# Kernel optimization log

Hardware: AMD Instinct MI355X
Metric: run time of the kernel (lower is better)

The kernel has to match this reference:

```python
import jax, jax.numpy as jnp
import numpy as np

S, B, D, H, DFF = 1024, 8, 1024, 16, 4096
HD = D // H
EPS = 1e-5


def layernorm(x, g, b):
    m = jnp.mean(x, axis=-1, keepdims=True)
    v = jnp.mean(jnp.square(x - m), axis=-1, keepdims=True)
    return (x - m) * jax.lax.rsqrt(v + EPS) * g + b


def setup_inputs() -> dict:
    key = jax.random.key(0)
    ks = jax.random.split(key, 6)
    w = 0.02
    return {
        "src": jax.random.normal(ks[0], (S, B, D), dtype=jnp.float32),
        "in_proj_w": jax.random.normal(ks[1], (3 * D, D), dtype=jnp.float32) * w,
        "in_proj_b": jnp.zeros((3 * D,), dtype=jnp.float32),
        "out_w": jax.random.normal(ks[2], (D, D), dtype=jnp.float32) * w,
        "out_b": jnp.zeros((D,), dtype=jnp.float32),
        "lin1_w": jax.random.normal(ks[3], (DFF, D), dtype=jnp.float32) * w,
        "lin1_b": jnp.zeros((DFF,), dtype=jnp.float32),
        "lin2_w": jax.random.normal(ks[4], (D, DFF), dtype=jnp.float32) * w,
        "lin2_b": jnp.zeros((D,), dtype=jnp.float32),
        "n1_g": jnp.ones((D,), dtype=jnp.float32),
        "n1_b": jnp.zeros((D,), dtype=jnp.float32),
        "n2_g": jnp.ones((D,), dtype=jnp.float32),
        "n2_b": jnp.zeros((D,), dtype=jnp.float32),
    }


def reference(src, in_proj_w, in_proj_b, out_w, out_b,
              lin1_w, lin1_b, lin2_w, lin2_b,
              n1_g, n1_b, n2_g, n2_b):
    # self-attention block (eval mode: dropout = identity)
    qkv = jnp.einsum('sbd,ed->sbe', src, in_proj_w) + in_proj_b  # [S,B,3D]
    q, k, v = jnp.split(qkv, 3, axis=-1)
    q = q.reshape(S, B, H, HD) * (1.0 / np.sqrt(HD)).astype(np.float32)
    k = k.reshape(S, B, H, HD)
    v = v.reshape(S, B, H, HD)
    scores = jnp.einsum('sbhd,tbhd->bhst', q, k)        # [B,H,S,S]
    attn = jax.nn.softmax(scores, axis=-1)
    o = jnp.einsum('bhst,tbhd->sbhd', attn, v).reshape(S, B, D)
    o = jnp.einsum('sbd,ed->sbe', o, out_w) + out_b
    # post-LN residuals
    x = layernorm(src + o, n1_g, n1_b)
    h = jax.nn.relu(jnp.einsum('sbd,fd->sbf', x, lin1_w) + lin1_b)
    f = jnp.einsum('sbf,df->sbd', h, lin2_w) + lin2_b
    return layernorm(x + f, n2_g, n2_b)
```

## Files before the change

kernel.cpp:

```cpp
#include <hip/hip_runtime.h>
#include <cstdint>
#include <cstddef>

#define S_  1024
#define B_  8
#define D_  1024
#define H_  16
#define HD_ 64
#define DFF_ 4096
#define M_  (S_*B_)
#define QKV_N (3*D_)

typedef float f32x4 __attribute__((ext_vector_type(4)));
typedef __bf16 bf16x8 __attribute__((ext_vector_type(8)));
typedef __bf16 bf16x4 __attribute__((ext_vector_type(4)));

#define GLDS16(gp, lp) __builtin_amdgcn_global_load_lds( \
    (__attribute__((address_space(1))) void*)(gp), \
    (__attribute__((address_space(3))) void*)(lp), 16, 0, 0)

#define CB0 (M_*D_/4)
#define CB1 (CB0 + QKV_N*D_/4)
#define CB2 (CB1 + D_*D_/4)
#define CB3 (CB2 + DFF_*D_/4)
#define CB4 (CB3 + D_*DFF_/4)

__global__ __launch_bounds__(256)
void cvt_all(const float* __restrict__ src, const float* __restrict__ w1f,
             const float* __restrict__ w2f, const float* __restrict__ w3f,
             const float* __restrict__ w4f,
             __bf16* __restrict__ src_bf, __bf16* __restrict__ w1,
             __bf16* __restrict__ w2, __bf16* __restrict__ w3,
             __bf16* __restrict__ w4)
{
    int i = blockIdx.x * 256 + threadIdx.x;
    const float* in; __bf16* out; int off;
    if      (i < CB0) { in = src; out = src_bf; off = 0;   }
    else if (i < CB1) { in = w1f; out = w1;     off = CB0; }
    else if (i < CB2) { in = w2f; out = w2;     off = CB1; }
    else if (i < CB3) { in = w3f; out = w3;     off = CB2; }
    else if (i < CB4) { in = w4f; out = w4;     off = CB3; }
    else return;
    int j = i - off;
    float4 v = *(const float4*)(in + (size_t)j * 4);
    __bf16 t[4] = {(__bf16)v.x, (__bf16)v.y, (__bf16)v.z, (__bf16)v.w};
    *(uint2*)(out + (size_t)j * 4) = *(uint2*)t;
}

template<bool OUT_BF16, bool RELU, bool ADD_BIAS, bool SPLITZ>
__global__ __launch_bounds__(512, 2)
void gemm256(const __bf16* __restrict__ A, const __bf16* __restrict__ W,
             const float* __restrict__ bias,
             void* __restrict__ Cv0, void* __restrict__ Cv1,
             int N, int Kloop, int lda)
{
    extern __shared__ __bf16 lds[];

    const int tid  = threadIdx.x;
    const int lane = tid & 63;
    const int wv   = tid >> 6;
    const int quad = lane >> 4;
    const int l15  = lane & 15;
    const int wm   = (wv >> 2) * 128;
    const int wn   = (wv & 3) * 64;

    const int id  = blockIdx.y * gridDim.x + blockIdx.x;
    const int nwg = gridDim.x * gridDim.y;
    const int q8  = nwg >> 3;
    const int k   = (id & 7) * q8 + (id >> 3);
    const int within = k & 31;
    const int chunk  = k >> 5;
    const int nchm   = gridDim.x >> 3;
    const int cm     = chunk % nchm;
    const int cn     = chunk / nchm;
    const int m0 = (cm * 8 + (within & 7)) * 256;
    const int n0 = (cn * 4 + (within >> 3)) * 256;

    void* Cv = Cv0;
    if (SPLITZ) {
        const int koff = blockIdx.z * Kloop;
        A += koff;
        W += koff;
        if (blockIdx.z) Cv = Cv1;
    }

    const int nt = Kloop >> 5;

    const int crow = tid >> 2;
    const int csl  = (tid & 3) ^ ((crow >> 1) & 3);
    const __bf16* gA0 = A + (size_t)(m0 + crow) * lda + csl * 8;
    const __bf16* gA1 = gA0 + (size_t)128 * lda;
    const __bf16* gW0 = W + (size_t)(n0 + crow) * lda + csl * 8;
    const __bf16* gW1 = gW0 + (size_t)128 * lda;
    char* ldsSt = (char*)lds + tid * 16;

    #define STAGE(kt, buf) do { \
        const int ko = (kt) << 5; \
        char* d_ = ldsSt + (buf) * 32768; \
        GLDS16(gW0 + ko, d_ + 16384); \
        GLDS16(gW1 + ko, d_ + 24576); \
        GLDS16(gA0 + ko, d_); \
        GLDS16(gA1 + ko, d_ + 8192); \
    } while (0)

    const int swz = (quad ^ ((l15 >> 1) & 3)) * 8;
    const __bf16* aBase = lds + (wm + l15) * 32 + swz;
    const __bf16* bBase = lds + 8192 + (wn + l15) * 32 + swz;

    #define RDA_ALL(arr, buf) do { const __bf16* p_ = aBase + (buf) * 16384; \
        _Pragma("unroll") for (int i_ = 0; i_ < 8; ++i_) \
            arr[i_] = *(const bf16x8*)(p_ + i_ * 512); } while (0)
    #define RDB_ALL(arr, buf) do { const __bf16* p_ = bBase + (buf) * 16384; \
        _Pragma("unroll") for (int j_ = 0; j_ < 4; ++j_) \
            arr[j_] = *(const bf16x8*)(p_ + j_ * 512); } while (0)

    #define BARRIER_DRAIN() do { \
        asm volatile("s_waitcnt vmcnt(0)" ::: "memory"); \
        __builtin_amdgcn_s_barrier(); \
        __builtin_amdgcn_sched_barrier(0); \
    } while (0)

    STAGE(0, 0);
    STAGE(1, 1);
    BARRIER_DRAIN();

    f32x4 acc[8][4] = {};
    bf16x8 aP[8], aN[8], b_[4];

    RDA_ALL(aP, 0);

    int b_cur = 0;
    for (int t = 0; t < nt; t += 2) {
        int b_nxt = b_cur + 1; if (b_nxt == 3) b_nxt = 0;
        int b_st  = b_nxt + 1; if (b_st  == 3) b_st  = 0;

        if (t + 2 < nt) STAGE(t + 2, b_st);
        RDB_ALL(b_, b_cur);
        RDA_ALL(aN, b_nxt);
        __builtin_amdgcn_s_setprio(1);
        #pragma unroll
        for (int i = 0; i < 8; ++i)
            #pragma unroll
            for (int j = 0; j < 4; ++j)
                acc[i][j] = __builtin_amdgcn_mfma_f32_16x16x32_bf16(aP[i], b_[j], acc[i][j], 0, 0, 0);
        __builtin_amdgcn_s_setprio(0);
        BARRIER_DRAIN();

        if (t + 3 < nt) STAGE(t + 3, b_cur);
        RDB_ALL(b_, b_nxt);
        if (t + 2 < nt) RDA_ALL(aP, b_st);
        __builtin_amdgcn_s_setprio(1);
        #pragma unroll
        for (int i = 0; i < 8; ++i)
            #pragma unroll
            for (int j = 0; j < 4; ++j)
                acc[i][j] = __builtin_amdgcn_mfma_f32_16x16x32_bf16(aN[i], b_[j], acc[i][j], 0, 0, 0);
        __builtin_amdgcn_s_setprio(0);
        if (t + 2 < nt) BARRIER_DRAIN();

        b_cur = b_st;
    }

    #undef BARRIER_DRAIN
    #undef RDA_ALL
    #undef RDB_ALL
    #undef STAGE

    float bvj[4];
    #pragma unroll
    for (int j = 0; j < 4; ++j)
        bvj[j] = ADD_BIAS ? bias[n0 + wn + j * 16 + l15] : 0.f;
    const size_t cbase = (size_t)(m0 + wm + quad * 4) * N + (n0 + wn + l15);
    #pragma unroll
    for (int i = 0; i < 8; ++i) {
        #pragma unroll
        for (int r = 0; r < 4; ++r) {
            const size_t rowb = cbase + (size_t)(i * 16 + r) * N;
            #pragma unroll
            for (int j = 0; j < 4; ++j) {
                float v = acc[i][j][r] + bvj[j];
                if (RELU) v = fmaxf(v, 0.f);
                if (OUT_BF16)
                    ((__bf16*)Cv)[rowb + j * 16] = (__bf16)v;
                else
                    ((float*)Cv)[rowb + j * 16] = v;
            }
        }
    }
}

__global__ __launch_bounds__(256)
void v_transpose(const __bf16* __restrict__ qkv, __bf16* __restrict__ vt)
{
    __shared__ __bf16 T[64 * 65];
    const int tid = threadIdx.x;
    const int t0  = blockIdx.x * 64;
    const int bh  = blockIdx.y;
    const int b   = bh & (B_ - 1);
    const int h   = bh / B_;

    #pragma unroll
    for (int j = 0; j < 2; ++j) {
        int c = j * 256 + tid;
        int i = c >> 3, cc = c & 7;
        const __bf16* g = qkv + (size_t)((t0 + i) * B_ + b) * QKV_N + 2 * D_ + h * HD_ + cc * 8;
        bf16x8 v = *(const bf16x8*)g;
        #pragma unroll
        for (int u = 0; u < 8; ++u) T[(cc * 8 + u) * 65 + i] = v[u];
    }
    __syncthreads();
    #pragma unroll
    for (int j = 0; j < 2; ++j) {
        int c = j * 256 + tid;
        int d = c >> 3, cc = c & 7;
        __bf16 pk[8];
        #pragma unroll
        for (int u = 0; u < 8; ++u) pk[u] = T[d * 65 + cc * 8 + u];
        *(uint4*)(vt + ((size_t)bh * HD_ + d) * S_ + t0 + cc * 8) = *(uint4*)pk;
    }
}

__global__ __launch_bounds__(512, 4)
void attn_flash(const __bf16* __restrict__ qkv, const __bf16* __restrict__ vt,
                __bf16* __restrict__ out)
{
    extern __shared__ __bf16 alds[];
    __bf16* Ks0 = alds;
    __bf16* Vs0 = alds + 16384;
    __bf16* Ps  = alds + 32768;

    const int tid  = threadIdx.x;
    const int lane = tid & 63;
    const int wv   = tid >> 6;
    const int quad = lane >> 4;
    const int l15  = lane & 15;

    const int id = blockIdx.y * gridDim.x + blockIdx.x;
    const int k  = (id & 7) * ((S_ / 128) * B_ * H_ / 8) + (id >> 3);
    const int s0 = (k & 7) * 128;
    const int bh = k >> 3;
    const int b  = bh & (B_ - 1);
    const int h  = bh / B_;

    const int i0k = tid >> 3, cck = tid & 7, scck = cck ^ (i0k & 7);
    const int i0v = tid >> 4, ccv = tid & 15, sccv = ccv ^ (i0v & 15);
    const __bf16* gK0 = qkv + ((size_t)i0k * B_ + b) * QKV_N + D_ + h * HD_ + scck * 8;
    const __bf16* gK1 = gK0 + (size_t)64 * B_ * QKV_N;
    const __bf16* gV0 = vt + ((size_t)bh * HD_ + i0v) * S_ + sccv * 8;
    const __bf16* gV1 = gV0 + (size_t)32 * S_;
    char* dK = (char*)Ks0 + tid * 16;
    char* dV = (char*)Vs0 + tid * 16;
    const size_t KADV = (size_t)128 * B_ * QKV_N;

    #define STAGEKV(buf) do { \
        GLDS16(gK0, dK + (buf) * 16384); \
        GLDS16(gK1, dK + (buf) * 16384 + 8192); \
        GLDS16(gV0, dV + (buf) * 16384); \
        GLDS16(gV1, dV + (buf) * 16384 + 8192); \
        gK0 += KADV; gK1 += KADV; gV0 += 128; gV1 += 128; \
    } while (0)

    STAGEKV(0);

    const int qrow = wv * 16 + l15;
    bf16x8 bq[2];
    #pragma unroll
    for (int kk = 0; kk < 2; ++kk)
        bq[kk] = *(const bf16x8*)(qkv + (size_t)((s0 + qrow) * B_ + b) * QKV_N
                                  + h * HD_ + kk * 32 + quad * 8);

    __syncthreads();

    f32x4 oacc[4] = {};
    float m_run = -1e30f, l_run = 0.f;
    const float C2    = 0.125f * 1.44269504f;
    const float LOG2E = 1.44269504f;
    const int xk = l15 & 7;
    const __bf16* psB = Ps + qrow * 64;

    const int nt2 = S_ / 128;
    for (int it = 0; it < nt2; ++it) {
        const int cur = it & 1;
        if (it + 1 < nt2) STAGEKV(cur ^ 1);

        #pragma unroll
        for (int s = 0; s < 2; ++s) {
            f32x4 sacc[4] = {};
            #pragma unroll
            for (int kk = 0; kk < 2; ++kk) {
                const __bf16* akB = Ks0 + cur * 8192 + s * 4096 + l15 * 64
                                    + (((kk * 4 + quad) ^ xk) * 8);
                #pragma unroll
                for (int j = 0; j < 4; ++j)
                    sacc[j] = __builtin_amdgcn_mfma_f32_16x16x32_bf16(
                        *(const bf16x8*)(akB + j * 1024), bq[kk], sacc[j], 0, 0, 0);
            }

            float mx = sacc[0][0];
            #pragma unroll
            for (int j = 0; j < 4; ++j)
                #pragma unroll
                for (int r = 0; r < 4; ++r) mx = fmaxf(mx, sacc[j][r]);
            mx = fmaxf(mx, __shfl_xor(mx, 16, 64));
            mx = fmaxf(mx, __shfl_xor(mx, 32, 64));
            float pm = mx * 0.125f;

            if (!__all(pm - m_run <= 8.0f)) {
                float mnew  = fmaxf(m_run, pm);
                float alpha = __builtin_amdgcn_exp2f((m_run - mnew) * LOG2E);
                l_run *= alpha;
                #pragma unroll
                for (int r = 0; r < 4; ++r) {
                    float ar = __shfl(alpha, quad * 4 + r, 64);
                    #pragma unroll
                    for (int jd = 0; jd < 4; ++jd) oacc[jd][r] *= ar;
                }
                m_run = mnew;
            }

            float k1 = m_run * LOG2E;
            float rs = 0.f;
            #pragma unroll
            for (int j = 0; j < 4; ++j)
                #pragma unroll
                for (int r = 0; r < 4; ++r) {
                    float p = __builtin_amdgcn_exp2f(sacc[j][r] * C2 - k1);
                    sacc[j][r] = p;
                    rs += p;
                }
            rs += __shfl_xor(rs, 16, 64);
            rs += __shfl_xor(rs, 32, 64);
            l_run += rs;

            #pragma unroll
            for (int j = 0; j < 4; ++j) {
                __bf16 pk[4] = {(__bf16)sacc[j][0], (__bf16)sacc[j][1],
                                (__bf16)sacc[j][2], (__bf16)sacc[j][3]};
                int s16 = (j * 2 + (quad >> 1)) ^ xk;
                *(uint2*)(psB + s16 * 8 + (quad & 1) * 4) = *(uint2*)pk;
            }

            #pragma unroll
            for (int kk = 0; kk < 2; ++kk) {
                bf16x8 ap = *(const bf16x8*)(psB + (((kk * 4 + quad) ^ xk) * 8));
                const __bf16* bvB = Vs0 + cur * 8192 + l15 * 128
                                    + (((s * 8 + kk * 4 + quad) ^ l15) * 8);
                #pragma unroll
                for (int jd = 0; jd < 4; ++jd)
                    oacc[jd] = __builtin_amdgcn_mfma_f32_16x16x32_bf16(
                        ap, *(const bf16x8*)(bvB + jd * 2048), oacc[jd], 0, 0, 0);
            }
        }

        __syncthreads();
    }
    #undef STAGEKV

    float linv = 1.f / l_run;
    #pragma unroll
    for (int r = 0; r < 4; ++r) {
        float lr = __shfl(linv, quad * 4 + r, 64);
        int s = s0 + wv * 16 + quad * 4 + r;
        #pragma unroll
        for (int jd = 0; jd < 4; ++jd) {
            int d = jd * 16 + l15;
            out[(size_t)(s * B_ + b) * D_ + h * HD_ + d] = (__bf16)(oacc[jd][r] * lr);
        }
    }
}

__global__ __launch_bounds__(256)
void ln_res3(const float* __restrict__ xa, const __bf16* __restrict__ p0,
             const __bf16* __restrict__ p1, const float* __restrict__ bias,
             const float* __restrict__ g, const float* __restrict__ beta,
             float* __restrict__ yout, __bf16* __restrict__ ybf)
{
    __shared__ float red[8];
    const int row = blockIdx.x;
    const int tid = threadIdx.x;
    const size_t base = (size_t)row * D_ + tid * 4;

    float4 a  = *(const float4*)(xa + base);
    bf16x4 q0 = *(const bf16x4*)(p0 + base);
    bf16x4 q1 = *(const bf16x4*)(p1 + base);
    float4 bb = *(const float4*)(bias + tid * 4);
    float x0 = a.x + (float)q0[0] + (float)q1[0] + bb.x;
    float x1 = a.y + (float)q0[1] + (float)q1[1] + bb.y;
    float x2 = a.z + (float)q0[2] + (float)q1[2] + bb.z;
    float x3 = a.w + (float)q0[3] + (float)q1[3] + bb.w;

    float s  = x0 + x1 + x2 + x3;
    float ss = x0 * x0 + x1 * x1 + x2 * x2 + x3 * x3;
    for (int msk = 1; msk <= 32; msk <<= 1) {
        s  += __shfl_xor(s,  msk, 64);
        ss += __shfl_xor(ss, msk, 64);
    }
    const int wv = tid >> 6;
    if ((tid & 63) == 0) { red[wv] = s; red[4 + wv] = ss; }
    __syncthreads();
    s  = red[0] + red[1] + red[2] + red[3];
    ss = red[4] + red[5] + red[6] + red[7];
    float mean = s * (1.f / D_);
    float var  = ss * (1.f / D_) - mean * mean;
    float rstd = rsqrtf(var + 1e-5f);

    float4 gv = *(const float4*)(g + tid * 4);
    float4 bv = *(const float4*)(beta + tid * 4);
    float y0 = (x0 - mean) * rstd * gv.x + bv.x;
    float y1 = (x1 - mean) * rstd * gv.y + bv.y;
    float y2 = (x2 - mean) * rstd * gv.z + bv.z;
    float y3 = (x3 - mean) * rstd * gv.w + bv.w;
    *(float4*)(yout + base) = make_float4(y0, y1, y2, y3);
    if (ybf) {
        __bf16 t[4] = {(__bf16)y0, (__bf16)y1, (__bf16)y2, (__bf16)y3};
        *(uint2*)(ybf + base) = *(uint2*)t;
    }
}

extern "C" void kernel_launch(void* const* d_in, const int* in_sizes, int n_in,
                              void* d_out, int out_size, void* d_ws, size_t ws_size,
                              hipStream_t stream)
{
    const float* src       = (const float*)d_in[0];
    const float* in_proj_w = (const float*)d_in[1];
    const float* in_proj_b = (const float*)d_in[2];
    const float* out_w     = (const float*)d_in[3];
    const float* out_b     = (const float*)d_in[4];
    const float* lin1_w    = (const float*)d_in[5];
    const float* lin1_b    = (const float*)d_in[6];
    const float* lin2_w    = (const float*)d_in[7];
    const float* lin2_b    = (const float*)d_in[8];
    const float* n1_g = (const float*)d_in[9];
    const float* n1_b = (const float*)d_in[10];
    const float* n2_g = (const float*)d_in[11];
    const float* n2_b = (const float*)d_in[12];

    char* ws = (char*)d_ws;
    size_t off = 0;
    auto alloc = [&](size_t bytes) { char* p = ws + off; off += (bytes + 255) & ~(size_t)255; return p; };

    __bf16* src_bf = (__bf16*)alloc((size_t)M_ * D_ * 2);
    __bf16* w1     = (__bf16*)alloc((size_t)QKV_N * D_ * 2);
    __bf16* w2     = (__bf16*)alloc((size_t)D_ * D_ * 2);
    __bf16* w3     = (__bf16*)alloc((size_t)DFF_ * D_ * 2);
    __bf16* w4     = (__bf16*)alloc((size_t)D_ * DFF_ * 2);
    __bf16* qkv    = (__bf16*)alloc((size_t)M_ * QKV_N * 2);
    char*   h_r    = alloc((size_t)M_ * DFF_ * 2);
    __bf16* xbf    = (__bf16*)alloc((size_t)M_ * D_ * 2);
    float*  xf     = (float*)alloc((size_t)M_ * D_ * 4);
    __bf16* vt     = (__bf16*)alloc((size_t)B_ * H_ * HD_ * S_ * 2);

    const size_t PART = (size_t)M_ * D_;
    __bf16* attn_o = src_bf;
    __bf16* o0 = (__bf16*)h_r;
    __bf16* o1 = o0 + PART;
    __bf16* hbf = (__bf16*)h_r;
    __bf16* f0 = vt;
    __bf16* f1 = xbf;

    const size_t SHM  = 98304;
    const size_t ASHM = 81920;

    cvt_all<<<(CB4 + 255) / 256, 256, 0, stream>>>(
        src, in_proj_w, out_w, lin1_w, lin2_w, src_bf, w1, w2, w3, w4);

    gemm256<true, false, true, false><<<dim3(M_ / 256, QKV_N / 256), 512, SHM, stream>>>(
        src_bf, w1, in_proj_b, qkv, nullptr, QKV_N, D_, D_);

    v_transpose<<<dim3(S_ / 64, B_ * H_), 256, 0, stream>>>(qkv, vt);

    attn_flash<<<dim3(S_ / 128, B_ * H_), 512, ASHM, stream>>>(qkv, vt, attn_o);

    gemm256<true, false, false, true><<<dim3(M_ / 256, D_ / 256, 2), 512, SHM, stream>>>(
        attn_o, w2, nullptr, o0, o1, D_, D_ / 2, D_);

    ln_res3<<<M_, 256, 0, stream>>>(src, o0, o1, out_b, n1_g, n1_b, xf, xbf);

    gemm256<true, true, true, false><<<dim3(M_ / 256, DFF_ / 256), 512, SHM, stream>>>(
        xbf, w3, lin1_b, hbf, nullptr, DFF_, D_, D_);

    gemm256<true, false, false, true><<<dim3(M_ / 256, D_ / 256, 2), 512, SHM, stream>>>(
        hbf, w4, nullptr, f0, f1, D_, DFF_ / 2, DFF_);

    ln_res3<<<M_, 256, 0, stream>>>(xf, f0, f1, lin2_b, n2_g, n2_b, (float*)d_out, nullptr);
}
```

Baseline: 457.0 us.

## Switch GEMM to four-buffer LDS ring with one barrier per two k-tiles

Replaces the triple-buffered GEMM main loop, which had a register double-buffered A prefetch and a barrier after every k-tile, with a 4-slot LDS ring. Two k-tiles are staged ahead at once and a single drain-and-barrier runs per pair of tiles. This halves the synchronisation count and simplifies register use. In exchange LDS per block grows from 96KB to 128KB, and fragment loads are no longer overlapped with the previous tile's MFMAs.

Measured after the change: 470.9 us. 1.03x slower.

```diff
diff --git a/kernel.cpp b/kernel.cpp
--- a/kernel.cpp
+++ b/kernel.cpp
@@ -94,9 +94,9 @@
     const __bf16* gW1 = gW0 + (size_t)128 * lda;
     char* ldsSt = (char*)lds + tid * 16;
 
-    #define STAGE(kt, buf) do { \
+    #define STAGE(kt) do { \
         const int ko = (kt) << 5; \
-        char* d_ = ldsSt + (buf) * 32768; \
+        char* d_ = ldsSt + (((kt) & 3) * 32768); \
         GLDS16(gW0 + ko, d_ + 16384); \
         GLDS16(gW1 + ko, d_ + 24576); \
         GLDS16(gA0 + ko, d_); \
@@ -107,63 +107,41 @@
     const __bf16* aBase = lds + (wm + l15) * 32 + swz;
     const __bf16* bBase = lds + 8192 + (wn + l15) * 32 + swz;
 
-    #define RDA_ALL(arr, buf) do { const __bf16* p_ = aBase + (buf) * 16384; \
+    #define TILE(kt) do { \
+        const __bf16* aB = aBase + ((kt) & 3) * 16384; \
+        const __bf16* bB = bBase + ((kt) & 3) * 16384; \
+        bf16x8 b_[4], a_[8]; \
+        _Pragma("unroll") for (int j_ = 0; j_ < 4; ++j_) \
+            b_[j_] = *(const bf16x8*)(bB + j_ * 512); \
         _Pragma("unroll") for (int i_ = 0; i_ < 8; ++i_) \
-            arr[i_] = *(const bf16x8*)(p_ + i_ * 512); } while (0)
-    #define RDB_ALL(arr, buf) do { const __bf16* p_ = bBase + (buf) * 16384; \
-        _Pragma("unroll") for (int j_ = 0; j_ < 4; ++j_) \
-            arr[j_] = *(const bf16x8*)(p_ + j_ * 512); } while (0)
-
-    #define BARRIER_DRAIN() do { \
-        asm volatile("s_waitcnt vmcnt(0)" ::: "memory"); \
-        __builtin_amdgcn_s_barrier(); \
-        __builtin_amdgcn_sched_barrier(0); \
+            a_[i_] = *(const bf16x8*)(aB + i_ * 512); \
+        __builtin_amdgcn_s_setprio(1); \
+        _Pragma("unroll") for (int i_ = 0; i_ < 8; ++i_) \
+            _Pragma("unroll") for (int j_ = 0; j_ < 4; ++j_) \
+                acc[i_][j_] = __builtin_amdgcn_mfma_f32_16x16x32_bf16(a_[i_], b_[j_], acc[i_][j_], 0, 0, 0); \
+        __builtin_amdgcn_s_setprio(0); \
     } while (0)
 
-    STAGE(0, 0);
-    STAGE(1, 1);
-    BARRIER_DRAIN();
+    STAGE(0);
+    STAGE(1);
+    asm volatile("s_waitcnt vmcnt(0)" ::: "memory");
+    __builtin_amdgcn_s_barrier();
+    __builtin_amdgcn_sched_barrier(0);
 
     f32x4 acc[8][4] = {};
-    bf16x8 aP[8], aN[8], b_[4];
-
-    RDA_ALL(aP, 0);
-
-    int b_cur = 0;
+
     for (int t = 0; t < nt; t += 2) {
-        int b_nxt = b_cur + 1; if (b_nxt == 3) b_nxt = 0;
-        int b_st  = b_nxt + 1; if (b_st  == 3) b_st  = 0;
-
-        if (t + 2 < nt) STAGE(t + 2, b_st);
-        RDB_ALL(b_, b_cur);
-        RDA_ALL(aN, b_nxt);
-        __builtin_amdgcn_s_setprio(1);
-        #pragma unroll
-        for (int i = 0; i < 8; ++i)
-            #pragma unroll
-            for (int j = 0; j < 4; ++j)
-                acc[i][j] = __builtin_amdgcn_mfma_f32_16x16x32_bf16(aP[i], b_[j], acc[i][j], 0, 0, 0);
-        __builtin_amdgcn_s_setprio(0);
-        BARRIER_DRAIN();
-
-        if (t + 3 < nt) STAGE(t + 3, b_cur);
-        RDB_ALL(b_, b_nxt);
-        if (t + 2 < nt) RDA_ALL(aP, b_st);
-        __builtin_amdgcn_s_setprio(1);
-        #pragma unroll
-        for (int i = 0; i < 8; ++i)
-            #pragma unroll
-            for (int j = 0; j < 4; ++j)
-                acc[i][j] = __builtin_amdgcn_mfma_f32_16x16x32_bf16(aN[i], b_[j], acc[i][j], 0, 0, 0);
-        __builtin_amdgcn_s_setprio(0);
-        if (t + 2 < nt) BARRIER_DRAIN();
-
-        b_cur = b_st;
-    }
-
-    #undef BARRIER_DRAIN
-    #undef RDA_ALL
-    #undef RDB_ALL
+        if (t + 2 < nt) { STAGE(t + 2); STAGE(t + 3); }
+        TILE(t);
+        TILE(t + 1);
+        if (t + 2 < nt) {
+            asm volatile("s_waitcnt vmcnt(0)" ::: "memory");
+            __builtin_amdgcn_s_barrier();
+            __builtin_amdgcn_sched_barrier(0);
+        }
+    }
+
+    #undef TILE
     #undef STAGE
 
     float bvj[4];
@@ -458,7 +436,7 @@
     __bf16* f0 = vt;
     __bf16* f1 = xbf;
 
-    const size_t SHM  = 98304;
+    const size_t SHM  = 131072;
     const size_t ASHM = 81920;
 
     cvt_all<<<(CB4 + 255) / 256, 256, 0, stream>>>(
```
